# Kernel optimization log

Hardware: AMD Instinct MI355X
Metric: run time of the kernel (lower is better)

The kernel has to match this reference:

```python
import jax, jax.numpy as jnp
import numpy as np

B, L, D, H = 4, 2048, 512, 8
HD = D // H  # 64
MAX_REL = 4


def setup_inputs() -> dict:
    key = jax.random.key(0)
    ks = jax.random.split(key, 13)
    s = 1.0 / np.sqrt(D)
    return {
        "q": jax.random.normal(ks[0], (B, L, D), jnp.float32),
        "k": jax.random.normal(ks[1], (B, L, D), jnp.float32),
        "v": jax.random.normal(ks[2], (B, L, D), jnp.float32),
        "Wq": jax.random.normal(ks[3], (D, D), jnp.float32) * s,
        "bq": jax.random.normal(ks[4], (D,), jnp.float32) * 0.01,
        "Wk": jax.random.normal(ks[5], (D, D), jnp.float32) * s,
        "bk": jax.random.normal(ks[6], (D,), jnp.float32) * 0.01,
        "Wv": jax.random.normal(ks[7], (D, D), jnp.float32) * s,
        "bv": jax.random.normal(ks[8], (D,), jnp.float32) * 0.01,
        "Wo": jax.random.normal(ks[9], (D, D), jnp.float32) * s,
        "bo": jax.random.normal(ks[10], (D,), jnp.float32) * 0.01,
        "rel_k_table": jax.random.normal(ks[11], (2 * MAX_REL + 1, HD), jnp.float32),
        "rel_v_table": jax.random.normal(ks[12], (2 * MAX_REL + 1, HD), jnp.float32),
    }


def _to_heads(x):
    # [B, L, D] -> [B, H, L, HD]
    b, l, d = x.shape
    return x.reshape(b, l, H, d // H).transpose(0, 2, 1, 3)


def reference(q, k, v, Wq, bq, Wk, bk, Wv, bv, Wo, bo, rel_k_table, rel_v_table):
    # NOTE: in the source, the relative-attention output is overwritten by the
    # plain SDPA call immediately after, so observable math = SDPA only.
    # rel_k_table / rel_v_table are dead parameters (zero gradient).
    relu = jax.nn.relu
    qh = _to_heads(relu(q @ Wq.T + bq))  # [B,H,L,HD]
    kh = _to_heads(relu(k @ Wk.T + bk))
    vh = _to_heads(relu(v @ Wv.T + bv))
    # scale by sqrt(d_key)=sqrt(512), matching the original (not sqrt(head_dim))
    scores = jnp.einsum("bhqd,bhkd->bhqk", qh, kh) / jnp.sqrt(jnp.float32(D))
    attn = jax.nn.softmax(scores, axis=-1)
    out = jnp.einsum("bhqk,bhkd->bhqd", attn, vh)  # [B,H,L,HD]
    out = out.transpose(0, 2, 1, 3).reshape(B, L, D)
    return relu(out @ Wo.T + bo)
```

## Files before the change

### kernel.cpp

```cpp
#include <hip/hip_runtime.h>
#include <hip/hip_bf16.h>

#define B_  4
#define L_  2048
#define D_  512
#define H_  8
#define HD_ 64
#define M_  (B_ * L_)

typedef __bf16 bf16;
typedef __attribute__((ext_vector_type(8)))  __bf16 bf16x8;
typedef __attribute__((ext_vector_type(4)))  __bf16 bf16x4;
typedef __attribute__((ext_vector_type(16))) float  f32x16;

__device__ __forceinline__ f32x16 mfma32(bf16x8 a, bf16x8 b, f32x16 c) {
    return __builtin_amdgcn_mfma_f32_32x32x16_bf16(a, b, c, 0, 0, 0);
}

__device__ __forceinline__ void pack_body(const float* __restrict__ src,
                                          bf16* __restrict__ dst, int R,
                                          int m0, int k0)
{
    __shared__ __align__(16) bf16 tile[64][76];
    const int t = threadIdx.x;
#pragma unroll
    for (int rep = 0; rep < 4; rep++) {
        const int idx = rep * 256 + t;
        const int r = idx >> 4, c4 = idx & 15;
        const float4 f = *(const float4*)(src + (size_t)(m0 + r) * 512 + k0 + c4 * 4);
        bf16x4 v; v[0] = (bf16)f.x; v[1] = (bf16)f.y; v[2] = (bf16)f.z; v[3] = (bf16)f.w;
        *(bf16x4*)(&tile[r][c4 * 4]) = v;
    }
    __syncthreads();
#pragma unroll
    for (int rep = 0; rep < 2; rep++) {
        const int s = rep * 256 + t;
        const int ml = s & 63, kpl = s >> 6;
        const bf16x4 lo = *(const bf16x4*)(&tile[ml][kpl * 8]);
        const bf16x4 hi4 = *(const bf16x4*)(&tile[ml][kpl * 8 + 4]);
        bf16x8 v;
#pragma unroll
        for (int e = 0; e < 4; e++) { v[e] = lo[e]; v[e + 4] = hi4[e]; }
        *(bf16x8*)(dst + ((size_t)(k0 / 8 + kpl) * R + m0 + ml) * 8) = v;
    }
}

__global__ __launch_bounds__(256) void pack_all(
    const float* __restrict__ q, const float* __restrict__ k,
    const float* __restrict__ v,
    const float* __restrict__ W0, const float* __restrict__ W1,
    const float* __restrict__ W2, const float* __restrict__ W3,
    bf16* __restrict__ Wp, bf16* __restrict__ P0, bf16* __restrict__ P1,
    bf16* __restrict__ P2)
{
    const int z = blockIdx.z;
    if (z < 4) {
        if (blockIdx.x >= 8) return;
        const float* src = z == 0 ? W0 : z == 1 ? W1 : z == 2 ? W2 : W3;
        pack_body(src, Wp + (size_t)z * 64 * 512 * 8, 512, blockIdx.x * 64, blockIdx.y * 64);
    } else {
        const float* src = z == 4 ? q : z == 5 ? k : v;
        bf16* dst = z == 4 ? P0 : z == 5 ? P1 : P2;
        pack_body(src, dst, M_, blockIdx.x * 64, blockIdx.y * 64);
    }
}

struct PJob {
    const bf16* X; const bf16* W; const float* bias; void* out;
    float postmul; int mode;
};

__global__ __launch_bounds__(256, 3) void proj_kernel(PJob j0, PJob j1, PJob j2)
{
    const PJob jb = (blockIdx.z == 0) ? j0 : (blockIdx.z == 1) ? j1 : j2;
    const int w    = threadIdx.x >> 6;
    const int lane = threadIdx.x & 63;
    const int l31  = lane & 31;
    const int hi   = lane >> 5;
    const int m0 = blockIdx.x * 128;
    const int n0 = blockIdx.y * 64;
    const int mh = w & 1;
    const int nh = w >> 1;

    __shared__ __align__(16) bf16 Ab[2][16][64][8];
    __shared__ __align__(16) bf16 Bb[2][8][64][8];

    f32x16 acc[2];
#pragma unroll
    for (int mi = 0; mi < 2; mi++)
#pragma unroll
        for (int r = 0; r < 16; r++) acc[mi][r] = 0.0f;

    auto ldA = [&](int f, int k0) -> bf16x8 {
        return *(const bf16x8*)(jb.X + ((size_t)((k0 >> 3) + (f >> 2) * 2 + hi) * M_
                                        + m0 + (f & 3) * 32 + l31) * 8);
    };
    auto ldB = [&](int f, int k0) -> bf16x8 {
        return *(const bf16x8*)(jb.W + ((size_t)((k0 >> 3) + (f >> 1) * 2 + hi) * 512
                                        + n0 + (f & 1) * 32 + l31) * 8);
    };

    bf16x8 rA[3][4], rB[3][2];
#pragma unroll
    for (int i = 0; i < 4; i++) rA[0][i] = ldA(w * 4 + i, 0);
#pragma unroll
    for (int i = 0; i < 2; i++) rB[0][i] = ldB(w * 2 + i, 0);
#pragma unroll
    for (int i = 0; i < 4; i++) *(bf16x8*)(&Ab[0][w * 4 + i][lane][0]) = rA[0][i];
#pragma unroll
    for (int i = 0; i < 2; i++) *(bf16x8*)(&Bb[0][w * 2 + i][lane][0]) = rB[0][i];
#pragma unroll
    for (int s = 1; s < 3; s++) {
#pragma unroll
        for (int i = 0; i < 4; i++) rA[s][i] = ldA(w * 4 + i, s * 64);
#pragma unroll
        for (int i = 0; i < 2; i++) rB[s][i] = ldB(w * 2 + i, s * 64);
    }
    __syncthreads();

#pragma unroll
    for (int it = 0; it < 8; it++) {
        const int cur = it & 1;
        if (it < 5) {
            const int s = it % 3, kn = (it + 3) * 64;
#pragma unroll
            for (int i = 0; i < 4; i++) rA[s][i] = ldA(w * 4 + i, kn);
#pragma unroll
            for (int i = 0; i < 2; i++) rB[s][i] = ldB(w * 2 + i, kn);
        }
#pragma unroll
        for (int ks = 0; ks < 4; ks++) {
            const bf16x8 bfr = *(const bf16x8*)(&Bb[cur][ks * 2 + nh][lane][0]);
#pragma unroll
            for (int mi = 0; mi < 2; mi++) {
                const bf16x8 afr = *(const bf16x8*)(&Ab[cur][ks * 4 + mh * 2 + mi][lane][0]);
                acc[mi] = mfma32(afr, bfr, acc[mi]);
            }
        }
        if (it < 7) {
            const int s = (it + 1) % 3;
#pragma unroll
            for (int i = 0; i < 4; i++) *(bf16x8*)(&Ab[1 - cur][w * 4 + i][lane][0]) = rA[s][i];
#pragma unroll
            for (int i = 0; i < 2; i++) *(bf16x8*)(&Bb[1 - cur][w * 2 + i][lane][0]) = rB[s][i];
            __syncthreads();
        }
    }

    const int col = n0 + nh * 32 + l31;
    const float bn = jb.bias[col];
    const int mode = jb.mode;
#pragma unroll
    for (int mi = 0; mi < 2; mi++)
#pragma unroll
        for (int r = 0; r < 16; r++) {
            const int row = m0 + (mh * 2 + mi) * 32 + (r & 3) + 8 * (r >> 2) + 4 * hi;
            float v = fmaxf(acc[mi][r] + bn, 0.0f);
            if (mode == 2) {
                ((float*)jb.out)[(size_t)row * D_ + col] = v;
            } else {
                v *= jb.postmul;
                const int b = row >> 11, l = row & (L_ - 1);
                const int h = col >> 6,  hd = col & (HD_ - 1);
                const int bh = b * H_ + h;
                size_t idx;
                if (mode == 0) {
                    idx = ((size_t)bh * L_ + l) * HD_ + hd;
                } else if (mode == 1) {
                    idx = (((size_t)bh * 8 + (hd >> 3)) * L_ + l) * 8 + (hd & 7);
                } else {
                    const int swzl = (l & ~15) | (l & 3) | ((l & 4) << 1) | ((l & 8) >> 1);
                    idx = (((size_t)bh * 256 + (swzl >> 3)) * 64 + hd) * 8 + (swzl & 7);
                }
                ((bf16*)jb.out)[idx] = (bf16)v;
            }
        }
}

__global__ __launch_bounds__(128, 2) void attn_kernel(
    const bf16* __restrict__ qh, const bf16* __restrict__ Kp,
    const bf16* __restrict__ Vp, bf16* __restrict__ Op)
{
    const int w    = threadIdx.x >> 6;
    const int lane = threadIdx.x & 63;
    const int l31  = lane & 31;
    const int hi   = lane >> 5;
    const int tw   = w * 16;

    const int lin  = blockIdx.x + (blockIdx.y << 6);
    const int xcd  = lin & 7;
    const int slot = lin >> 3;
    const int bh   = (xcd << 2) + (slot >> 6);
    const int qb   = (slot & 63) << 5;

    const bf16* Q   = qh + (size_t)bh * L_ * HD_;
    const bf16* Kpb = Kp + (size_t)bh * 8 * L_ * 8;
    const bf16* Vpb = Vp + (size_t)bh * 256 * 64 * 8;

    __shared__ __align__(16) float sm[3][64][16];

    bf16x8 qf[4];
#pragma unroll
    for (int ks = 0; ks < 4; ks++)
        qf[ks] = *(const bf16x8*)(Q + (size_t)(qb + l31) * HD_ + ks * 16 + hi * 8);

    f32x16 zz;
#pragma unroll
    for (int r = 0; r < 16; r++) zz[r] = 0.0f;
    f32x16 o0 = zz, o1 = zz, lacc = zz;
    bf16x8 ones;
#pragma unroll
    for (int u = 0; u < 8; u++) ones[u] = (bf16)1.0f;

    auto ldK = [&](int f, int t) -> bf16x8 {
        return *(const bf16x8*)(Kpb + ((size_t)((f >> 1) * 2 + hi) * L_
                                       + t * 64 + (f & 1) * 32 + l31) * 8);
    };
    auto ldV = [&](int f, int t) -> bf16x8 {
        return *(const bf16x8*)(Vpb + ((size_t)(t * 8 + (f >> 1) * 2 + hi) * 64
                                       + (f & 1) * 32 + l31) * 8);
    };

    bf16x8 kr[8], vf[8];
#pragma unroll
    for (int f = 0; f < 8; f++) kr[f] = ldK(f, tw);
#pragma unroll
    for (int f = 0; f < 8; f++) vf[f] = ldV(f, tw);

#pragma unroll 2
    for (int tt = 0; tt < 16; tt++) {
        const int t = tw + tt;
        __builtin_amdgcn_s_setprio(1);
        f32x16 s0 = mfma32(kr[0], qf[0], zz);
        f32x16 s1 = mfma32(kr[1], qf[0], zz);
#pragma unroll
        for (int ks = 1; ks < 4; ks++) {
            s0 = mfma32(kr[ks * 2 + 0], qf[ks], s0);
            s1 = mfma32(kr[ks * 2 + 1], qf[ks], s1);
        }
        __builtin_amdgcn_s_setprio(0);
        if (tt < 15) {
#pragma unroll
            for (int f = 0; f < 8; f++) kr[f] = ldK(f, t + 1);
        }

#pragma unroll
        for (int r = 0; r < 16; r++) s0[r] = __builtin_amdgcn_exp2f(s0[r]);
        bf16x8 pf0, pf1;
#pragma unroll
        for (int u = 0; u < 8; u++) { pf0[u] = (bf16)s0[u]; pf1[u] = (bf16)s0[8 + u]; }
        __builtin_amdgcn_s_setprio(1);
        o0   = mfma32(pf0, vf[0], o0);
        o1   = mfma32(pf0, vf[1], o1);
        lacc = mfma32(pf0, ones, lacc);
        o0   = mfma32(pf1, vf[2], o0);
        o1   = mfma32(pf1, vf[3], o1);
        lacc = mfma32(pf1, ones, lacc);
        __builtin_amdgcn_s_setprio(0);
        if (tt < 15) {
#pragma unroll
            for (int f = 0; f < 4; f++) vf[f] = ldV(f, t + 1);
        }

#pragma unroll
        for (int r = 0; r < 16; r++) s1[r] = __builtin_amdgcn_exp2f(s1[r]);
        bf16x8 pf2, pf3;
#pragma unroll
        for (int u = 0; u < 8; u++) { pf2[u] = (bf16)s1[u]; pf3[u] = (bf16)s1[8 + u]; }
        __builtin_amdgcn_s_setprio(1);
        o0   = mfma32(pf2, vf[4], o0);
        o1   = mfma32(pf2, vf[5], o1);
        lacc = mfma32(pf2, ones, lacc);
        o0   = mfma32(pf3, vf[6], o0);
        o1   = mfma32(pf3, vf[7], o1);
        lacc = mfma32(pf3, ones, lacc);
        __builtin_amdgcn_s_setprio(0);
        if (tt < 15) {
#pragma unroll
            for (int f = 4; f < 8; f++) vf[f] = ldV(f, t + 1);
        }
    }

    if (w == 1) {
        *(f32x16*)(&sm[0][lane][0]) = o0;
        *(f32x16*)(&sm[1][lane][0]) = o1;
        *(f32x16*)(&sm[2][lane][0]) = lacc;
    }
    __syncthreads();
    if (w == 1) return;
    {
        const f32x16 a0 = *(const f32x16*)(&sm[0][lane][0]);
        const f32x16 a1 = *(const f32x16*)(&sm[1][lane][0]);
        const f32x16 al = *(const f32x16*)(&sm[2][lane][0]);
#pragma unroll
        for (int r = 0; r < 16; r++) {
            o0[r] += a0[r]; o1[r] += a1[r]; lacc[r] += al[r];
        }
    }

    const int b = bh >> 3, h = bh & 7;
#pragma unroll
    for (int r = 0; r < 16; r++) {
        const int rl = (r & 3) + 8 * (r >> 2) + 4 * hi;
        const float inv = 1.0f / lacc[r];
        const int m = b * L_ + qb + rl;
        const int c0 = h * HD_ + l31;
        Op[((size_t)(c0 >> 3) * M_ + m) * 8 + (c0 & 7)] = (bf16)(o0[r] * inv);
        const int c1 = c0 + 32;
        Op[((size_t)(c1 >> 3) * M_ + m) * 8 + (c1 & 7)] = (bf16)(o1[r] * inv);
    }
}

extern "C" void kernel_launch(void* const* d_in, const int* in_sizes, int n_in,
                              void* d_out, int out_size, void* d_ws, size_t ws_size,
                              hipStream_t stream)
{
    (void)in_sizes; (void)n_in; (void)out_size;
    const float* q  = (const float*)d_in[0];
    const float* k  = (const float*)d_in[1];
    const float* v  = (const float*)d_in[2];
    const float* Wq = (const float*)d_in[3];
    const float* bq = (const float*)d_in[4];
    const float* Wk = (const float*)d_in[5];
    const float* bk = (const float*)d_in[6];
    const float* Wv = (const float*)d_in[7];
    const float* bv = (const float*)d_in[8];
    const float* Wo = (const float*)d_in[9];
    const float* bo = (const float*)d_in[10];
    float* out = (float*)d_out;

    char* ws = (char*)d_ws;
    const size_t MB = 1024 * 1024;
    bf16* P0  = (bf16*)(ws);
    bf16* P1  = (bf16*)(ws + 8 * MB);
    bf16* P2  = (bf16*)(ws + 16 * MB);
    bf16* Wp  = (bf16*)(ws + 24 * MB);
    bf16* qh  = (bf16*)(d_out);
    bf16* Kp  = (bf16*)((char*)d_out + 8 * MB);
    bf16* Opb = P1;

    bf16* Wqp = Wp;
    bf16* Wkp = Wp + (size_t)64 * 512 * 8;
    bf16* Wvp = Wp + (size_t)2 * 64 * 512 * 8;
    bf16* Wop = Wp + (size_t)3 * 64 * 512 * 8;

    const float SCALE_LOG2E = 0.06377946282349575f;

    dim3 pb(256);
    pack_all<<<dim3(128, 8, 7), pb, 0, stream>>>(q, k, v, Wq, Wk, Wv, Wo,
                                                 Wp, P0, P1, P2);

    if (ws_size >= (size_t)34 * MB) {
        bf16* VpN = (bf16*)(ws + 26 * MB);
        PJob jq{P0, Wqp, bq, qh,  SCALE_LOG2E, 0};
        PJob jk{P1, Wkp, bk, Kp,  1.0f, 1};
        PJob jv{P2, Wvp, bv, VpN, 1.0f, 3};
        proj_kernel<<<dim3(64, 8, 3), pb, 0, stream>>>(jq, jk, jv);

        attn_kernel<<<dim3(64, 32), dim3(128), 0, stream>>>(qh, Kp, VpN, Opb);
    } else {
        bf16* Vp = P0;
        PJob jq{P0, Wqp, bq, qh, SCALE_LOG2E, 0};
        PJob jk{P1, Wkp, bk, Kp, 1.0f, 1};
        proj_kernel<<<dim3(64, 8, 2), pb, 0, stream>>>(jq, jk, jk);

        PJob jv{P2, Wvp, bv, Vp, 1.0f, 3};
        proj_kernel<<<dim3(64, 8, 1), pb, 0, stream>>>(jv, jv, jv);

        attn_kernel<<<dim3(64, 32), dim3(128), 0, stream>>>(qh, Kp, Vp, Opb);
    }

    PJob jo{Opb, Wop, bo, out, 1.0f, 2};
    proj_kernel<<<dim3(64, 8, 1), pb, 0, stream>>>(jo, jo, jo);
}
```

Baseline: 202.5 us.

## Replace ones-MFMA row-sum with scalar sum, reorder S/PV interleave, raise occupancy

The softmax denominator was computed by extra MFMAs against a ones vector, with a 16-register accumulator. It is now summed in VALU per lane and combined across the half-waves with shuffles at the end. The loop now interleaves QK^T for the two key halves with the PV MFMAs, so only one score accumulator is live at a time. Launch bounds rise to 3 waves/SIMD and the LDS reduction layout becomes conflict-free. This removes a third of the PV MFMA work and frees registers for occupancy, but adds VALU adds and may cause spills under the tighter register budget.

```diff
diff --git a/kernel.cpp b/kernel.cpp
--- a/kernel.cpp
+++ b/kernel.cpp
@@ -177,7 +177,7 @@
         }
 }
 
-__global__ __launch_bounds__(128, 2) void attn_kernel(
+__global__ __launch_bounds__(128, 3) void attn_kernel(
     const bf16* __restrict__ qh, const bf16* __restrict__ Kp,
     const bf16* __restrict__ Vp, bf16* __restrict__ Op)
 {
@@ -197,7 +197,8 @@
     const bf16* Kpb = Kp + (size_t)bh * 8 * L_ * 8;
     const bf16* Vpb = Vp + (size_t)bh * 256 * 64 * 8;
 
-    __shared__ __align__(16) float sm[3][64][16];
+    __shared__ float smo[2][16][64];
+    __shared__ float sml[64];
 
     bf16x8 qf[4];
 #pragma unroll
@@ -207,10 +208,8 @@
     f32x16 zz;
 #pragma unroll
     for (int r = 0; r < 16; r++) zz[r] = 0.0f;
-    f32x16 o0 = zz, o1 = zz, lacc = zz;
-    bf16x8 ones;
-#pragma unroll
-    for (int u = 0; u < 8; u++) ones[u] = (bf16)1.0f;
+    f32x16 o0 = zz, o1 = zz;
+    float ls = 0.0f;
 
     auto ldK = [&](int f, int t) -> bf16x8 {
         return *(const bf16x8*)(Kpb + ((size_t)((f >> 1) * 2 + hi) * L_
@@ -230,50 +229,63 @@
 #pragma unroll 2
     for (int tt = 0; tt < 16; tt++) {
         const int t = tw + tt;
+
         __builtin_amdgcn_s_setprio(1);
         f32x16 s0 = mfma32(kr[0], qf[0], zz);
-        f32x16 s1 = mfma32(kr[1], qf[0], zz);
-#pragma unroll
-        for (int ks = 1; ks < 4; ks++) {
-            s0 = mfma32(kr[ks * 2 + 0], qf[ks], s0);
-            s1 = mfma32(kr[ks * 2 + 1], qf[ks], s1);
-        }
+#pragma unroll
+        for (int ks = 1; ks < 4; ks++) s0 = mfma32(kr[ks * 2], qf[ks], s0);
+        __builtin_amdgcn_s_setprio(0);
+
+#pragma unroll
+        for (int r = 0; r < 16; r++) s0[r] = __builtin_amdgcn_exp2f(s0[r]);
+        {
+            float a0 = (s0[0] + s0[1]) + (s0[2] + s0[3]);
+            float a1 = (s0[4] + s0[5]) + (s0[6] + s0[7]);
+            float a2 = (s0[8] + s0[9]) + (s0[10] + s0[11]);
+            float a3 = (s0[12] + s0[13]) + (s0[14] + s0[15]);
+            ls += (a0 + a1) + (a2 + a3);
+        }
+        bf16x8 pf0, pf1;
+#pragma unroll
+        for (int u = 0; u < 8; u++) { pf0[u] = (bf16)s0[u]; pf1[u] = (bf16)s0[8 + u]; }
+        __builtin_amdgcn_s_setprio(1);
+        o0 = mfma32(pf0, vf[0], o0);
+        o1 = mfma32(pf0, vf[1], o1);
+        o0 = mfma32(pf1, vf[2], o0);
+        o1 = mfma32(pf1, vf[3], o1);
         __builtin_amdgcn_s_setprio(0);
         if (tt < 15) {
 #pragma unroll
-            for (int f = 0; f < 8; f++) kr[f] = ldK(f, t + 1);
-        }
-
-#pragma unroll
-        for (int r = 0; r < 16; r++) s0[r] = __builtin_amdgcn_exp2f(s0[r]);
-        bf16x8 pf0, pf1;
-#pragma unroll
-        for (int u = 0; u < 8; u++) { pf0[u] = (bf16)s0[u]; pf1[u] = (bf16)s0[8 + u]; }
+            for (int f = 0; f < 4; f++) vf[f] = ldV(f, t + 1);
+        }
+
         __builtin_amdgcn_s_setprio(1);
-        o0   = mfma32(pf0, vf[0], o0);
-        o1   = mfma32(pf0, vf[1], o1);
-        lacc = mfma32(pf0, ones, lacc);
-        o0   = mfma32(pf1, vf[2], o0);
-        o1   = mfma32(pf1, vf[3], o1);
-        lacc = mfma32(pf1, ones, lacc);
+        f32x16 s1 = mfma32(kr[1], qf[0], zz);
+#pragma unroll
+        for (int ks = 1; ks < 4; ks++) s1 = mfma32(kr[ks * 2 + 1], qf[ks], s1);
         __builtin_amdgcn_s_setprio(0);
         if (tt < 15) {
 #pragma unroll
-            for (int f = 0; f < 4; f++) vf[f] = ldV(f, t + 1);
+            for (int f = 0; f < 8; f++) kr[f] = ldK(f, t + 1);
         }
 
 #pragma unroll
         for (int r = 0; r < 16; r++) s1[r] = __builtin_amdgcn_exp2f(s1[r]);
+        {
+            float a0 = (s1[0] + s1[1]) + (s1[2] + s1[3]);
+            float a1 = (s1[4] + s1[5]) + (s1[6] + s1[7]);
+            float a2 = (s1[8] + s1[9]) + (s1[10] + s1[11]);
+            float a3 = (s1[12] + s1[13]) + (s1[14] + s1[15]);
+            ls += (a0 + a1) + (a2 + a3);
+        }
         bf16x8 pf2, pf3;
 #pragma unroll
         for (int u = 0; u < 8; u++) { pf2[u] = (bf16)s1[u]; pf3[u] = (bf16)s1[8 + u]; }
         __builtin_amdgcn_s_setprio(1);
-        o0   = mfma32(pf2, vf[4], o0);
-        o1   = mfma32(pf2, vf[5], o1);
-        lacc = mfma32(pf2, ones, lacc);
-        o0   = mfma32(pf3, vf[6], o0);
-        o1   = mfma32(pf3, vf[7], o1);
-        lacc = mfma32(pf3, ones, lacc);
+        o0 = mfma32(pf2, vf[4], o0);
+        o1 = mfma32(pf2, vf[5], o1);
+        o0 = mfma32(pf3, vf[6], o0);
+        o1 = mfma32(pf3, vf[7], o1);
         __builtin_amdgcn_s_setprio(0);
         if (tt < 15) {
 #pragma unroll
@@ -282,27 +294,29 @@
     }
 
     if (w == 1) {
-        *(f32x16*)(&sm[0][lane][0]) = o0;
-        *(f32x16*)(&sm[1][lane][0]) = o1;
-        *(f32x16*)(&sm[2][lane][0]) = lacc;
+#pragma unroll
+        for (int r = 0; r < 16; r++) {
+            smo[0][r][lane] = o0[r];
+            smo[1][r][lane] = o1[r];
+        }
+        sml[lane] = ls;
     }
     __syncthreads();
     if (w == 1) return;
-    {
-        const f32x16 a0 = *(const f32x16*)(&sm[0][lane][0]);
-        const f32x16 a1 = *(const f32x16*)(&sm[1][lane][0]);
-        const f32x16 al = *(const f32x16*)(&sm[2][lane][0]);
-#pragma unroll
-        for (int r = 0; r < 16; r++) {
-            o0[r] += a0[r]; o1[r] += a1[r]; lacc[r] += al[r];
-        }
-    }
+#pragma unroll
+    for (int r = 0; r < 16; r++) {
+        o0[r] += smo[0][r][lane];
+        o1[r] += smo[1][r][lane];
+    }
+    ls += sml[lane];
+
+    const float lst = ls + __shfl_xor(ls, 32);
 
     const int b = bh >> 3, h = bh & 7;
 #pragma unroll
     for (int r = 0; r < 16; r++) {
         const int rl = (r & 3) + 8 * (r >> 2) + 4 * hi;
-        const float inv = 1.0f / lacc[r];
+        const float inv = 1.0f / __shfl(lst, rl);
         const int m = b * L_ + qb + rl;
         const int c0 = h * HD_ + l31;
         Op[((size_t)(c0 >> 3) * M_ + m) * 8 + (c0 & 7)] = (bf16)(o0[r] * inv);
```

After: 462.3 us. 128% more time.
